# Kernel tuning notes

Measured on AMD Instinct MI355X. Metric: run time of the kernel, lower is better.

Reference implementation:

```python
import jax, jax.numpy as jnp
import numpy as np

# attn_reps = "8x0n+30x1n": per head channel C = 8 scalars + 30 Lorentz four-vectors (4 each) = 128
N_SCALARS, N_VECTORS = 8, 30
ETA = jnp.diag(jnp.array([1.0, -1.0, -1.0, -1.0], dtype=jnp.float32))  # Minkowski metric


def _quat_to_rot(q):
    # q: (M,4) unit quaternions -> (M,3,3) rotation matrices
    w, x, y, z = q[:, 0], q[:, 1], q[:, 2], q[:, 3]
    r0 = jnp.stack([1 - 2 * (y * y + z * z), 2 * (x * y - w * z), 2 * (x * z + w * y)], axis=-1)
    r1 = jnp.stack([2 * (x * y + w * z), 1 - 2 * (x * x + z * z), 2 * (y * z - w * x)], axis=-1)
    r2 = jnp.stack([2 * (x * z - w * y), 2 * (y * z + w * x), 1 - 2 * (x * x + y * y)], axis=-1)
    return jnp.stack([r0, r1, r2], axis=-2)


def _random_lorentz(key, M):
    # random proper Lorentz transforms: boost(beta) @ blockdiag(1, R)
    k1, k2 = jax.random.split(key)
    quat = jax.random.normal(k1, (M, 4), dtype=jnp.float32)
    quat = quat / jnp.linalg.norm(quat, axis=-1, keepdims=True)
    R = _quat_to_rot(quat)  # (M,3,3)
    beta = jax.random.uniform(k2, (M, 3), minval=-1.0, maxval=1.0, dtype=jnp.float32) * (0.6 / np.sqrt(3.0))
    b2 = jnp.sum(beta * beta, axis=-1)  # (M,), < 0.36
    gamma = 1.0 / jnp.sqrt(1.0 - b2)
    n = beta / jnp.sqrt(jnp.maximum(b2, 1e-12))[:, None]
    gb = gamma[:, None] * beta  # (M,3)
    top = jnp.concatenate([gamma[:, None], gb], axis=-1)[:, None, :]  # (M,1,4)
    spatial = jnp.eye(3, dtype=jnp.float32) + (gamma - 1.0)[:, None, None] * n[:, :, None] * n[:, None, :]
    bottom = jnp.concatenate([gb[:, :, None], spatial], axis=-1)  # (M,3,4)
    B = jnp.concatenate([top, bottom], axis=-2)  # (M,4,4) boost
    rot4 = jnp.zeros((M, 4, 4), dtype=jnp.float32).at[:, 0, 0].set(1.0).at[:, 1:, 1:].set(R)
    return jnp.einsum('mij,mjk->mik', B, rot4)


def setup_inputs() -> dict:
    key = jax.random.key(0)
    kq, kk, kv, kl = jax.random.split(key, 4)
    B, H, N, C = 8, 8, 1024, 128
    q = jax.random.normal(kq, (B, H, N, C), dtype=jnp.float32)
    k = jax.random.normal(kk, (B, H, N, C), dtype=jnp.float32)
    v = jax.random.normal(kv, (B, H, N, C), dtype=jnp.float32)
    L = _random_lorentz(kl, B * N).reshape(B, N, 4, 4)
    return {"q_local": q, "k_local": k, "v_local": v, "lframes_matrices": L}


def _transform(x, M):
    # TensorRepsTransform: scalars pass through, four-vectors get v' = M v (per particle)
    # x: (B,H,N,C), M: (B,N,4,4)
    s = x[..., :N_SCALARS]
    vec = x[..., N_SCALARS:].reshape(x.shape[:-1] + (N_VECTORS, 4))
    vec = jnp.einsum('bnij,bhnvj->bhnvi', M, vec)
    return jnp.concatenate([s, vec.reshape(x.shape[:-1] + (N_VECTORS * 4,))], axis=-1)


def reference(q_local, k_local, v_local, lframes_matrices):
    C = q_local.shape[-1]
    # InverseLFrames: Lorentz inverse  Lambda^{-1} = eta Lambda^T eta
    inv = jnp.einsum('ij,bnkj,kl->bnil', ETA, lframes_matrices, ETA)
    # LowerIndices: lower the output index -> eta @ Lambda^{-1}
    lower_inv = jnp.einsum('ij,bnjk->bnik', ETA, inv)
    q_g = _transform(q_local, inv)
    k_g = _transform(k_local, lower_inv)
    v_g = _transform(v_local, inv)
    # standard SDPA (scale 1/sqrt(C))
    scores = jnp.einsum('bhqc,bhkc->bhqk', q_g, k_g) * (1.0 / np.sqrt(C))
    attn = jax.nn.softmax(scores, axis=-1)
    out_g = jnp.einsum('bhqk,bhkc->bhqc', attn, v_g)
    # back to local frame with Lambda itself
    return _transform(out_g, lframes_matrices)
```

## Files before the change

kernel.cpp:

```cpp
#include <hip/hip_runtime.h>

typedef _Float16 f16;
typedef _Float16 f16x4 __attribute__((ext_vector_type(4)));
typedef _Float16 f16x8 __attribute__((ext_vector_type(8)));
typedef float    f32x4 __attribute__((ext_vector_type(4)));

#define NSEQ 1024
#define CD   128
#define QT   64
#define KT   64
#define LQ   136
#define LV   72

__global__ __launch_bounds__(256)
void ipa_pre(const float* __restrict__ kg, const float* __restrict__ vg,
             const float* __restrict__ Lm, f16* __restrict__ kh, f16* __restrict__ vh)
{
    __shared__ float LL[64 * 16];
    const int bh = blockIdx.x, nt = blockIdx.y, b = bh >> 3, tid = threadIdx.x;
    const float* Lb = Lm + ((size_t)b * NSEQ + nt * 64) * 16;
    for (int t = tid; t < 64 * 16; t += 256) LL[t] = Lb[t];
    __syncthreads();
    const size_t base = ((size_t)bh * NSEQ + nt * 64) * CD;
    #pragma unroll
    for (int it = 0; it < 8; ++it) {
        int g = it * 256 + tid;
        int row = g >> 5, cg = g & 31;
        size_t idx = base + row * CD + cg * 4;
        const float* Lr = &LL[row * 16];
        float4 xk = *(const float4*)(kg + idx);
        float4 xv = *(const float4*)(vg + idx);
        float4 yk = xk, yv = xv;
        if (cg >= 2) {
            float t0 = xk.x, t1 = -xk.y, t2 = -xk.z, t3 = -xk.w;
            yk.x = Lr[0]*t0 + Lr[4]*t1 + Lr[8] *t2 + Lr[12]*t3;
            yk.y = Lr[1]*t0 + Lr[5]*t1 + Lr[9] *t2 + Lr[13]*t3;
            yk.z = Lr[2]*t0 + Lr[6]*t1 + Lr[10]*t2 + Lr[14]*t3;
            yk.w = Lr[3]*t0 + Lr[7]*t1 + Lr[11]*t2 + Lr[15]*t3;
            t0 = xv.x; t1 = -xv.y; t2 = -xv.z; t3 = -xv.w;
            yv.x =  (Lr[0]*t0 + Lr[4]*t1 + Lr[8] *t2 + Lr[12]*t3);
            yv.y = -(Lr[1]*t0 + Lr[5]*t1 + Lr[9] *t2 + Lr[13]*t3);
            yv.z = -(Lr[2]*t0 + Lr[6]*t1 + Lr[10]*t2 + Lr[14]*t3);
            yv.w = -(Lr[3]*t0 + Lr[7]*t1 + Lr[11]*t2 + Lr[15]*t3);
        }
        f16x4 hk = {(f16)yk.x, (f16)yk.y, (f16)yk.z, (f16)yk.w};
        f16x4 hv = {(f16)yv.x, (f16)yv.y, (f16)yv.z, (f16)yv.w};
        *(f16x4*)(kh + idx) = hk;
        *(f16x4*)(vh + idx) = hv;
    }
}

__global__ __launch_bounds__(256, 4)
void ipa_attn(const float* __restrict__ qg, const f16* __restrict__ kh,
              const f16* __restrict__ vh, const float* __restrict__ Lm,
              float* __restrict__ out)
{
    __shared__ __align__(16) f16 Ks[KT * LQ];
    __shared__ __align__(16) f16 Vt[CD * LV];

    const int tid  = threadIdx.x;
    const int bh   = blockIdx.x, qt = blockIdx.y, b = bh >> 3;
    const int lane = tid & 63, w = tid >> 6, lq = lane & 15, quad = lane >> 4;
    const int q0   = qt * QT;

    float* LL = (float*)Vt;
    const float* Lqb = Lm + ((size_t)b * NSEQ + q0) * 16;
    for (int t = tid; t < 64 * 16; t += 256) LL[t] = Lqb[t];
    __syncthreads();

    const float sc = 0.08838834764831845f;
    const size_t qbase = ((size_t)bh * NSEQ + q0) * CD;
    #pragma unroll
    for (int it = 0; it < 8; ++it) {
        int g = it * 256 + tid;
        int row = g >> 5, cg = g & 31;
        float4 x = *(const float4*)(qg + qbase + row * CD + cg * 4);
        const float* Lr = &LL[row * 16];
        float4 y = x;
        if (cg >= 2) {
            float t0 = x.x, t1 = -x.y, t2 = -x.z, t3 = -x.w;
            y.x =  (Lr[0]*t0 + Lr[4]*t1 + Lr[8] *t2 + Lr[12]*t3);
            y.y = -(Lr[1]*t0 + Lr[5]*t1 + Lr[9] *t2 + Lr[13]*t3);
            y.z = -(Lr[2]*t0 + Lr[6]*t1 + Lr[10]*t2 + Lr[14]*t3);
            y.w = -(Lr[3]*t0 + Lr[7]*t1 + Lr[11]*t2 + Lr[15]*t3);
        }
        f16x4 h = {(f16)(y.x*sc), (f16)(y.y*sc), (f16)(y.z*sc), (f16)(y.w*sc)};
        *(f16x4*)&Ks[row * LQ + cg * 4] = h;
    }
    __syncthreads();

    f16x8 qf[4];
    #pragma unroll
    for (int cs = 0; cs < 4; ++cs)
        qf[cs] = *(const f16x8*)&Ks[(w * 16 + lq) * LQ + cs * 32 + quad * 8];

    f32x4 oacc[8];
    #pragma unroll
    for (int cb = 0; cb < 8; ++cb) oacc[cb] = (f32x4){0.f, 0.f, 0.f, 0.f};
    float mrun = -1e30f, lrun = 0.0f;

    const size_t kvbase = (size_t)bh * NSEQ * CD;

    for (int kt0 = 0; kt0 < NSEQ; kt0 += KT) {
        __syncthreads();

        #pragma unroll
        for (int it = 0; it < 4; ++it) {
            int ch = it * 256 + tid;
            int m = ch >> 4, c0 = (ch & 15) * 8;
            int gg = m >> 5, mm = m & 31;
            int h = (mm >> 4) & 1, a = (mm >> 2) & 3, r = mm & 3;
            int kap = gg * 32 + 8 * a + 4 * h + r;
            f16x8 kv8 = *(const f16x8*)(kh + kvbase + (size_t)(kt0 + kap) * CD + c0);
            *(f16x8*)&Ks[m * LQ + c0] = kv8;
        }
        {
            int key = tid & 63, wv = tid >> 6;
            #pragma unroll
            for (int j = 0; j < 4; ++j) {
                int c0 = wv * 32 + j * 8;
                f16x8 vv = *(const f16x8*)(vh + kvbase + (size_t)(kt0 + key) * CD + c0);
                #pragma unroll
                for (int i = 0; i < 8; ++i) Vt[(c0 + i) * LV + key] = vv[i];
            }
        }
        __syncthreads();

        #pragma unroll
        for (int g2 = 0; g2 < 2; ++g2) {
            f32x4 s0 = (f32x4){0.f,0.f,0.f,0.f}, s1 = (f32x4){0.f,0.f,0.f,0.f};
            #pragma unroll
            for (int cs = 0; cs < 4; ++cs) {
                f16x8 ka = *(const f16x8*)&Ks[(g2 * 32 + lq)      * LQ + cs * 32 + quad * 8];
                f16x8 kb = *(const f16x8*)&Ks[(g2 * 32 + 16 + lq) * LQ + cs * 32 + quad * 8];
                s0 = __builtin_amdgcn_mfma_f32_16x16x32_f16(ka, qf[cs], s0, 0, 0, 0);
                s1 = __builtin_amdgcn_mfma_f32_16x16x32_f16(kb, qf[cs], s1, 0, 0, 0);
            }
            float mx = fmaxf(fmaxf(fmaxf(s0.x,s0.y), fmaxf(s0.z,s0.w)),
                             fmaxf(fmaxf(s1.x,s1.y), fmaxf(s1.z,s1.w)));
            mx = fmaxf(mx, __shfl_xor(mx, 16, 64));
            mx = fmaxf(mx, __shfl_xor(mx, 32, 64));
            float mnew  = fmaxf(mrun, mx);
            float alpha = __expf(mrun - mnew);
            float p0=__expf(s0.x-mnew), p1=__expf(s0.y-mnew), p2=__expf(s0.z-mnew), p3=__expf(s0.w-mnew);
            float p4=__expf(s1.x-mnew), p5=__expf(s1.y-mnew), p6=__expf(s1.z-mnew), p7=__expf(s1.w-mnew);
            float rs = ((p0+p1)+(p2+p3)) + ((p4+p5)+(p6+p7));
            rs += __shfl_xor(rs, 16, 64);
            rs += __shfl_xor(rs, 32, 64);
            lrun = alpha * lrun + rs;
            mrun = mnew;
            f16x8 pf = {(f16)p0,(f16)p1,(f16)p2,(f16)p3,(f16)p4,(f16)p5,(f16)p6,(f16)p7};
            #pragma unroll
            for (int cb = 0; cb < 8; ++cb) {
                f16x8 vf = *(const f16x8*)&Vt[(cb * 16 + lq) * LV + g2 * 32 + quad * 8];
                oacc[cb] *= alpha;
                oacc[cb] = __builtin_amdgcn_mfma_f32_16x16x32_f16(vf, pf, oacc[cb], 0, 0, 0);
            }
        }
    }

    float invl = 1.0f / lrun;
    const int qrow = w * 16 + lq;
    const float* Lr = Lm + ((size_t)b * NSEQ + q0 + qrow) * 16;
    float* ob = out + ((size_t)bh * NSEQ + q0 + qrow) * CD;
    #pragma unroll
    for (int cb = 0; cb < 8; ++cb) {
        int c0 = cb * 16 + quad * 4;
        float o0 = oacc[cb].x*invl, o1 = oacc[cb].y*invl, o2 = oacc[cb].z*invl, o3 = oacc[cb].w*invl;
        float4 r;
        if (c0 >= 8) {
            r.x = Lr[0] *o0 + Lr[1] *o1 + Lr[2] *o2 + Lr[3] *o3;
            r.y = Lr[4] *o0 + Lr[5] *o1 + Lr[6] *o2 + Lr[7] *o3;
            r.z = Lr[8] *o0 + Lr[9] *o1 + Lr[10]*o2 + Lr[11]*o3;
            r.w = Lr[12]*o0 + Lr[13]*o1 + Lr[14]*o2 + Lr[15]*o3;
        } else {
            r.x = o0; r.y = o1; r.z = o2; r.w = o3;
        }
        *(float4*)(ob + c0) = r;
    }
}

extern "C" void kernel_launch(void* const* d_in, const int* in_sizes, int n_in,
                              void* d_out, int out_size, void* d_ws, size_t ws_size,
                              hipStream_t stream) {
    const float* q = (const float*)d_in[0];
    const float* k = (const float*)d_in[1];
    const float* v = (const float*)d_in[2];
    const float* L = (const float*)d_in[3];
    float* o = (float*)d_out;
    f16* kh = (f16*)d_ws;
    f16* vh = kh + (size_t)64 * NSEQ * CD;
    dim3 grid(64, NSEQ / KT);
    ipa_pre<<<grid, 256, 0, stream>>>(k, v, L, kh, vh);
    dim3 grid2(64, NSEQ / QT);
    ipa_attn<<<grid2, 256, 0, stream>>>(q, kh, vh, L, o);
}
```

Baseline: 212.4 us.

## Enlarge attention tiles to 128x128, precompute Q in pre-pass, XOR-swizzle LDS

Q transformation and f16 conversion move into the pre-pass kernel, so the attention kernel loads ready f16 Q fragments straight from global memory. Each wave now handles 32 query rows (two 16-row MFMA groups) against 128-key tiles. Every K and V fragment read from shared memory is reused for two query groups, and there are half as many tile iterations and barriers. Padded LDS layouts are replaced by XOR swizzles to avoid bank conflicts. The cost is higher register pressure (occupancy hint lowered to 2), more LDS per block, half as many blocks, and an extra global round trip for Q.

Measured after the change: 211.5 us. About the same (-0.4%).

```diff
diff --git a/kernel.cpp b/kernel.cpp
--- a/kernel.cpp
+++ b/kernel.cpp
@@ -7,14 +7,13 @@
 
 #define NSEQ 1024
 #define CD   128
-#define QT   64
-#define KT   64
-#define LQ   136
-#define LV   72
+#define QT   128
+#define KT   128
 
 __global__ __launch_bounds__(256)
-void ipa_pre(const float* __restrict__ kg, const float* __restrict__ vg,
-             const float* __restrict__ Lm, f16* __restrict__ kh, f16* __restrict__ vh)
+void ipa_pre(const float* __restrict__ qg, const float* __restrict__ kg,
+             const float* __restrict__ vg, const float* __restrict__ Lm,
+             f16* __restrict__ qh, f16* __restrict__ kh, f16* __restrict__ vh)
 {
     __shared__ float LL[64 * 16];
     const int bh = blockIdx.x, nt = blockIdx.y, b = bh >> 3, tid = threadIdx.x;
@@ -22,15 +21,17 @@
     for (int t = tid; t < 64 * 16; t += 256) LL[t] = Lb[t];
     __syncthreads();
     const size_t base = ((size_t)bh * NSEQ + nt * 64) * CD;
+    const float sc = 0.08838834764831845f;
     #pragma unroll
     for (int it = 0; it < 8; ++it) {
         int g = it * 256 + tid;
         int row = g >> 5, cg = g & 31;
         size_t idx = base + row * CD + cg * 4;
         const float* Lr = &LL[row * 16];
+        float4 xq = *(const float4*)(qg + idx);
         float4 xk = *(const float4*)(kg + idx);
         float4 xv = *(const float4*)(vg + idx);
-        float4 yk = xk, yv = xv;
+        float4 yq = xq, yk = xk, yv = xv;
         if (cg >= 2) {
             float t0 = xk.x, t1 = -xk.y, t2 = -xk.z, t3 = -xk.w;
             yk.x = Lr[0]*t0 + Lr[4]*t1 + Lr[8] *t2 + Lr[12]*t3;
@@ -42,141 +43,160 @@
             yv.y = -(Lr[1]*t0 + Lr[5]*t1 + Lr[9] *t2 + Lr[13]*t3);
             yv.z = -(Lr[2]*t0 + Lr[6]*t1 + Lr[10]*t2 + Lr[14]*t3);
             yv.w = -(Lr[3]*t0 + Lr[7]*t1 + Lr[11]*t2 + Lr[15]*t3);
-        }
+            t0 = xq.x; t1 = -xq.y; t2 = -xq.z; t3 = -xq.w;
+            yq.x =  (Lr[0]*t0 + Lr[4]*t1 + Lr[8] *t2 + Lr[12]*t3);
+            yq.y = -(Lr[1]*t0 + Lr[5]*t1 + Lr[9] *t2 + Lr[13]*t3);
+            yq.z = -(Lr[2]*t0 + Lr[6]*t1 + Lr[10]*t2 + Lr[14]*t3);
+            yq.w = -(Lr[3]*t0 + Lr[7]*t1 + Lr[11]*t2 + Lr[15]*t3);
+        }
+        f16x4 hq = {(f16)(yq.x*sc), (f16)(yq.y*sc), (f16)(yq.z*sc), (f16)(yq.w*sc)};
         f16x4 hk = {(f16)yk.x, (f16)yk.y, (f16)yk.z, (f16)yk.w};
         f16x4 hv = {(f16)yv.x, (f16)yv.y, (f16)yv.z, (f16)yv.w};
+        *(f16x4*)(qh + idx) = hq;
         *(f16x4*)(kh + idx) = hk;
         *(f16x4*)(vh + idx) = hv;
     }
 }
 
-__global__ __launch_bounds__(256, 4)
-void ipa_attn(const float* __restrict__ qg, const f16* __restrict__ kh,
+__global__ __launch_bounds__(256, 2)
+void ipa_attn(const f16* __restrict__ qh, const f16* __restrict__ kh,
               const f16* __restrict__ vh, const float* __restrict__ Lm,
               float* __restrict__ out)
 {
-    __shared__ __align__(16) f16 Ks[KT * LQ];
-    __shared__ __align__(16) f16 Vt[CD * LV];
+    __shared__ __align__(16) f16 Ks[KT * CD];
+    __shared__ __align__(16) f16 Vt[CD * KT];
 
     const int tid  = threadIdx.x;
     const int bh   = blockIdx.x, qt = blockIdx.y, b = bh >> 3;
     const int lane = tid & 63, w = tid >> 6, lq = lane & 15, quad = lane >> 4;
     const int q0   = qt * QT;
-
-    float* LL = (float*)Vt;
-    const float* Lqb = Lm + ((size_t)b * NSEQ + q0) * 16;
-    for (int t = tid; t < 64 * 16; t += 256) LL[t] = Lqb[t];
-    __syncthreads();
-
-    const float sc = 0.08838834764831845f;
-    const size_t qbase = ((size_t)bh * NSEQ + q0) * CD;
-    #pragma unroll
-    for (int it = 0; it < 8; ++it) {
-        int g = it * 256 + tid;
-        int row = g >> 5, cg = g & 31;
-        float4 x = *(const float4*)(qg + qbase + row * CD + cg * 4);
-        const float* Lr = &LL[row * 16];
-        float4 y = x;
-        if (cg >= 2) {
-            float t0 = x.x, t1 = -x.y, t2 = -x.z, t3 = -x.w;
-            y.x =  (Lr[0]*t0 + Lr[4]*t1 + Lr[8] *t2 + Lr[12]*t3);
-            y.y = -(Lr[1]*t0 + Lr[5]*t1 + Lr[9] *t2 + Lr[13]*t3);
-            y.z = -(Lr[2]*t0 + Lr[6]*t1 + Lr[10]*t2 + Lr[14]*t3);
-            y.w = -(Lr[3]*t0 + Lr[7]*t1 + Lr[11]*t2 + Lr[15]*t3);
-        }
-        f16x4 h = {(f16)(y.x*sc), (f16)(y.y*sc), (f16)(y.z*sc), (f16)(y.w*sc)};
-        *(f16x4*)&Ks[row * LQ + cg * 4] = h;
-    }
-    __syncthreads();
-
-    f16x8 qf[4];
-    #pragma unroll
-    for (int cs = 0; cs < 4; ++cs)
-        qf[cs] = *(const f16x8*)&Ks[(w * 16 + lq) * LQ + cs * 32 + quad * 8];
-
-    f32x4 oacc[8];
-    #pragma unroll
-    for (int cb = 0; cb < 8; ++cb) oacc[cb] = (f32x4){0.f, 0.f, 0.f, 0.f};
-    float mrun = -1e30f, lrun = 0.0f;
-
     const size_t kvbase = (size_t)bh * NSEQ * CD;
+
+    f16x8 qf[2][4];
+    #pragma unroll
+    for (int u = 0; u < 2; ++u)
+        #pragma unroll
+        for (int cs = 0; cs < 4; ++cs)
+            qf[u][cs] = *(const f16x8*)(qh + kvbase + (size_t)(q0 + w*32 + u*16 + lq) * CD
+                                           + cs * 32 + quad * 8);
+
+    f32x4 oacc[2][8];
+    #pragma unroll
+    for (int u = 0; u < 2; ++u)
+        #pragma unroll
+        for (int cb = 0; cb < 8; ++cb) oacc[u][cb] = (f32x4){0.f, 0.f, 0.f, 0.f};
+    float mrun[2] = {-1e30f, -1e30f}, lrun[2] = {0.f, 0.f};
 
     for (int kt0 = 0; kt0 < NSEQ; kt0 += KT) {
         __syncthreads();
 
         #pragma unroll
-        for (int it = 0; it < 4; ++it) {
-            int ch = it * 256 + tid;
-            int m = ch >> 4, c0 = (ch & 15) * 8;
-            int gg = m >> 5, mm = m & 31;
-            int h = (mm >> 4) & 1, a = (mm >> 2) & 3, r = mm & 3;
-            int kap = gg * 32 + 8 * a + 4 * h + r;
-            f16x8 kv8 = *(const f16x8*)(kh + kvbase + (size_t)(kt0 + kap) * CD + c0);
-            *(f16x8*)&Ks[m * LQ + c0] = kv8;
-        }
-        {
-            int key = tid & 63, wv = tid >> 6;
-            #pragma unroll
-            for (int j = 0; j < 4; ++j) {
-                int c0 = wv * 32 + j * 8;
-                f16x8 vv = *(const f16x8*)(vh + kvbase + (size_t)(kt0 + key) * CD + c0);
-                #pragma unroll
-                for (int i = 0; i < 8; ++i) Vt[(c0 + i) * LV + key] = vv[i];
-            }
+        for (int it = 0; it < 8; ++it) {
+            int g = it * 256 + tid;
+            int m = g >> 4, c0 = (g & 15) * 8;
+            int mm = m & 31, h = (mm >> 4) & 1, a = (mm >> 2) & 3, r = mm & 3;
+            int kap = (m & ~31) | (8 * a + 4 * h + r);
+            f16x8 kv = *(const f16x8*)(kh + kvbase + (size_t)(kt0 + kap) * CD + c0);
+            *(f16x8*)&Ks[m * CD + (c0 ^ ((m & 7) << 3))] = kv;
+        }
+        #pragma unroll
+        for (int j = 0; j < 8; ++j) {
+            int key = (tid & 63) + (j & 1) * 64;
+            int c0  = (tid >> 6) * 32 + (j >> 1) * 8;
+            f16x8 vv = *(const f16x8*)(vh + kvbase + (size_t)(kt0 + key) * CD + c0);
+            #pragma unroll
+            for (int i = 0; i < 8; ++i)
+                Vt[(c0 + i) * KT + (key ^ (i << 3))] = vv[i];
         }
         __syncthreads();
 
         #pragma unroll
-        for (int g2 = 0; g2 < 2; ++g2) {
-            f32x4 s0 = (f32x4){0.f,0.f,0.f,0.f}, s1 = (f32x4){0.f,0.f,0.f,0.f};
-            #pragma unroll
-            for (int cs = 0; cs < 4; ++cs) {
-                f16x8 ka = *(const f16x8*)&Ks[(g2 * 32 + lq)      * LQ + cs * 32 + quad * 8];
-                f16x8 kb = *(const f16x8*)&Ks[(g2 * 32 + 16 + lq) * LQ + cs * 32 + quad * 8];
-                s0 = __builtin_amdgcn_mfma_f32_16x16x32_f16(ka, qf[cs], s0, 0, 0, 0);
-                s1 = __builtin_amdgcn_mfma_f32_16x16x32_f16(kb, qf[cs], s1, 0, 0, 0);
-            }
-            float mx = fmaxf(fmaxf(fmaxf(s0.x,s0.y), fmaxf(s0.z,s0.w)),
-                             fmaxf(fmaxf(s1.x,s1.y), fmaxf(s1.z,s1.w)));
-            mx = fmaxf(mx, __shfl_xor(mx, 16, 64));
-            mx = fmaxf(mx, __shfl_xor(mx, 32, 64));
-            float mnew  = fmaxf(mrun, mx);
-            float alpha = __expf(mrun - mnew);
-            float p0=__expf(s0.x-mnew), p1=__expf(s0.y-mnew), p2=__expf(s0.z-mnew), p3=__expf(s0.w-mnew);
-            float p4=__expf(s1.x-mnew), p5=__expf(s1.y-mnew), p6=__expf(s1.z-mnew), p7=__expf(s1.w-mnew);
-            float rs = ((p0+p1)+(p2+p3)) + ((p4+p5)+(p6+p7));
-            rs += __shfl_xor(rs, 16, 64);
-            rs += __shfl_xor(rs, 32, 64);
-            lrun = alpha * lrun + rs;
-            mrun = mnew;
-            f16x8 pf = {(f16)p0,(f16)p1,(f16)p2,(f16)p3,(f16)p4,(f16)p5,(f16)p6,(f16)p7};
-            #pragma unroll
-            for (int cb = 0; cb < 8; ++cb) {
-                f16x8 vf = *(const f16x8*)&Vt[(cb * 16 + lq) * LV + g2 * 32 + quad * 8];
-                oacc[cb] *= alpha;
-                oacc[cb] = __builtin_amdgcn_mfma_f32_16x16x32_f16(vf, pf, oacc[cb], 0, 0, 0);
+        for (int half = 0; half < 2; ++half) {
+            const int kb = half * 64;
+            f32x4 s[2][4];
+            #pragma unroll
+            for (int u = 0; u < 2; ++u)
+                #pragma unroll
+                for (int g = 0; g < 4; ++g) s[u][g] = (f32x4){0.f, 0.f, 0.f, 0.f};
+            #pragma unroll
+            for (int g = 0; g < 4; ++g) {
+                int R = kb + g * 16 + lq;
+                #pragma unroll
+                for (int cs = 0; cs < 4; ++cs) {
+                    f16x8 ka = *(const f16x8*)&Ks[R * CD + ((cs*32 + quad*8) ^ ((R & 7) << 3))];
+                    s[0][g] = __builtin_amdgcn_mfma_f32_16x16x32_f16(ka, qf[0][cs], s[0][g], 0, 0, 0);
+                    s[1][g] = __builtin_amdgcn_mfma_f32_16x16x32_f16(ka, qf[1][cs], s[1][g], 0, 0, 0);
+                }
+            }
+            f16x8 pf[2][2];
+            float alpha[2];
+            #pragma unroll
+            for (int u = 0; u < 2; ++u) {
+                float mx = -1e30f;
+                #pragma unroll
+                for (int g = 0; g < 4; ++g)
+                    mx = fmaxf(mx, fmaxf(fmaxf(s[u][g].x, s[u][g].y), fmaxf(s[u][g].z, s[u][g].w)));
+                mx = fmaxf(mx, __shfl_xor(mx, 16, 64));
+                mx = fmaxf(mx, __shfl_xor(mx, 32, 64));
+                float mnew = fmaxf(mrun[u], mx);
+                alpha[u] = __expf(mrun[u] - mnew);
+                float rs = 0.f;
+                float p[16];
+                #pragma unroll
+                for (int g = 0; g < 4; ++g) {
+                    p[g*4+0] = __expf(s[u][g].x - mnew);
+                    p[g*4+1] = __expf(s[u][g].y - mnew);
+                    p[g*4+2] = __expf(s[u][g].z - mnew);
+                    p[g*4+3] = __expf(s[u][g].w - mnew);
+                    rs += (p[g*4+0] + p[g*4+1]) + (p[g*4+2] + p[g*4+3]);
+                }
+                rs += __shfl_xor(rs, 16, 64);
+                rs += __shfl_xor(rs, 32, 64);
+                lrun[u] = alpha[u] * lrun[u] + rs;
+                mrun[u] = mnew;
+                pf[u][0] = (f16x8){(f16)p[0],(f16)p[1],(f16)p[2],(f16)p[3],(f16)p[4],(f16)p[5],(f16)p[6],(f16)p[7]};
+                pf[u][1] = (f16x8){(f16)p[8],(f16)p[9],(f16)p[10],(f16)p[11],(f16)p[12],(f16)p[13],(f16)p[14],(f16)p[15]};
+            }
+            #pragma unroll
+            for (int u = 0; u < 2; ++u)
+                #pragma unroll
+                for (int cb = 0; cb < 8; ++cb) oacc[u][cb] *= alpha[u];
+            #pragma unroll
+            for (int p2 = 0; p2 < 2; ++p2) {
+                int kbase = kb + p2 * 32 + quad * 8;
+                #pragma unroll
+                for (int cb = 0; cb < 8; ++cb) {
+                    int c = cb * 16 + lq;
+                    f16x8 vf = *(const f16x8*)&Vt[c * KT + (kbase ^ ((c & 7) << 3))];
+                    oacc[0][cb] = __builtin_amdgcn_mfma_f32_16x16x32_f16(vf, pf[0][p2], oacc[0][cb], 0, 0, 0);
+                    oacc[1][cb] = __builtin_amdgcn_mfma_f32_16x16x32_f16(vf, pf[1][p2], oacc[1][cb], 0, 0, 0);
+                }
             }
         }
     }
 
-    float invl = 1.0f / lrun;
-    const int qrow = w * 16 + lq;
-    const float* Lr = Lm + ((size_t)b * NSEQ + q0 + qrow) * 16;
-    float* ob = out + ((size_t)bh * NSEQ + q0 + qrow) * CD;
-    #pragma unroll
-    for (int cb = 0; cb < 8; ++cb) {
-        int c0 = cb * 16 + quad * 4;
-        float o0 = oacc[cb].x*invl, o1 = oacc[cb].y*invl, o2 = oacc[cb].z*invl, o3 = oacc[cb].w*invl;
-        float4 r;
-        if (c0 >= 8) {
-            r.x = Lr[0] *o0 + Lr[1] *o1 + Lr[2] *o2 + Lr[3] *o3;
-            r.y = Lr[4] *o0 + Lr[5] *o1 + Lr[6] *o2 + Lr[7] *o3;
-            r.z = Lr[8] *o0 + Lr[9] *o1 + Lr[10]*o2 + Lr[11]*o3;
-            r.w = Lr[12]*o0 + Lr[13]*o1 + Lr[14]*o2 + Lr[15]*o3;
-        } else {
-            r.x = o0; r.y = o1; r.z = o2; r.w = o3;
-        }
-        *(float4*)(ob + c0) = r;
+    #pragma unroll
+    for (int u = 0; u < 2; ++u) {
+        const int qrow = w * 32 + u * 16 + lq;
+        float invl = 1.0f / lrun[u];
+        const float* Lr = Lm + ((size_t)b * NSEQ + q0 + qrow) * 16;
+        float* ob = out + ((size_t)bh * NSEQ + q0 + qrow) * CD;
+        #pragma unroll
+        for (int cb = 0; cb < 8; ++cb) {
+            int c0 = cb * 16 + quad * 4;
+            float o0 = oacc[u][cb].x*invl, o1 = oacc[u][cb].y*invl;
+            float o2 = oacc[u][cb].z*invl, o3 = oacc[u][cb].w*invl;
+            float4 r;
+            if (c0 >= 8) {
+                r.x = Lr[0] *o0 + Lr[1] *o1 + Lr[2] *o2 + Lr[3] *o3;
+                r.y = Lr[4] *o0 + Lr[5] *o1 + Lr[6] *o2 + Lr[7] *o3;
+                r.z = Lr[8] *o0 + Lr[9] *o1 + Lr[10]*o2 + Lr[11]*o3;
+                r.w = Lr[12]*o0 + Lr[13]*o1 + Lr[14]*o2 + Lr[15]*o3;
+            } else {
+                r.x = o0; r.y = o1; r.z = o2; r.w = o3;
+            }
+            *(float4*)(ob + c0) = r;
+        }
     }
 }
 
@@ -188,10 +208,12 @@
     const float* v = (const float*)d_in[2];
     const float* L = (const float*)d_in[3];
     float* o = (float*)d_out;
-    f16* kh = (f16*)d_ws;
-    f16* vh = kh + (size_t)64 * NSEQ * CD;
-    dim3 grid(64, NSEQ / KT);
-    ipa_pre<<<grid, 256, 0, stream>>>(k, v, L, kh, vh);
+    const size_t tot = (size_t)64 * NSEQ * CD;
+    f16* qh = (f16*)d_ws;
+    f16* kh = qh + tot;
+    f16* vh = kh + tot;
+    dim3 grid1(64, NSEQ / 64);
+    ipa_pre<<<grid1, 256, 0, stream>>>(q, k, v, L, qh, kh, vh);
     dim3 grid2(64, NSEQ / QT);
-    ipa_attn<<<grid2, 256, 0, stream>>>(q, kh, vh, L, o);
+    ipa_attn<<<grid2, 256, 0, stream>>>(qh, kh, vh, L, o);
 }
```
